# Performance work log

Measured on AMD Instinct MI355X. Metric: run time of the kernel, lower is better.

Reference implementation:

```python
import jax, jax.numpy as jnp
import numpy as np

# Graph sizes: each graph has exactly 32 nodes (forced by the rearrange + lin1 in_features)
BS = 4096
NODES = 32
N = BS * NODES          # 131072 total nodes
F_IN = 128
E_PER_G = 512
E = BS * E_PER_G        # 2097152 edges, all within-graph
HID = 1024
NCLS = 10


def setup_inputs() -> dict:
    key = jax.random.key(0)
    ks = jax.random.split(key, 9)
    x = jax.random.normal(ks[0], (N, F_IN), dtype=jnp.float32)
    # within-graph random edges: local node ids in [0,32) + per-graph offset
    graph_off = jnp.repeat(jnp.arange(BS, dtype=jnp.int64), E_PER_G) * NODES
    src = jax.random.randint(ks[1], (E,), 0, NODES, dtype=jnp.int64) + graph_off
    dst = jax.random.randint(ks[2], (E,), 0, NODES, dtype=jnp.int64) + graph_off
    edge_index = jnp.stack([src, dst], axis=0)
    s = 0.05
    gconv_w = jax.random.normal(ks[3], (F_IN, F_IN), dtype=jnp.float32) * s
    gconv_b = jax.random.normal(ks[4], (F_IN,), dtype=jnp.float32) * s
    lin1_w = jax.random.normal(ks[5], (HID, F_IN * NODES), dtype=jnp.float32) * s
    lin1_b = jax.random.normal(ks[6], (HID,), dtype=jnp.float32) * s
    lin2_w = jax.random.normal(ks[7], (NCLS, HID), dtype=jnp.float32) * s
    lin2_b = jax.random.normal(ks[8], (NCLS,), dtype=jnp.float32) * s
    return {"x": x, "edge_index": edge_index, "gconv_w": gconv_w,
            "gconv_b": gconv_b, "lin1_w": lin1_w, "lin1_b": lin1_b,
            "lin2_w": lin2_w, "lin2_b": lin2_b, "bs": BS}


def reference(x, edge_index, gconv_w, gconv_b, lin1_w, lin1_b, lin2_w, lin2_b, bs):
    # GINConv (eps=0): h_i = Linear( x_i + sum_{j->i} x_j )
    src, dst = edge_index[0], edge_index[1]
    agg = jax.ops.segment_sum(x[src], dst, num_segments=x.shape[0])  # [N, F]
    h = (x + agg) @ gconv_w.T + gconv_b                               # [N, F]
    h = jax.nn.relu(h)
    # rearrange '(bs e) f -> bs (f e)' with e=32 nodes per graph
    f = h.shape[-1]
    h = h.reshape(bs, NODES, f).transpose(0, 2, 1).reshape(bs, f * NODES)
    h = h @ lin1_w.T + lin1_b
    # dropout is identity in eval mode
    h = jax.nn.relu(h)
    h = h @ lin2_w.T + lin2_b
    return jax.nn.softmax(h, axis=-1)
```

## Files before the change

kernel.cpp:

```cpp
#include <hip/hip_runtime.h>

typedef _Float16 half_t;
typedef _Float16 halfv8 __attribute__((ext_vector_type(8)));
typedef _Float16 halfv4 __attribute__((ext_vector_type(4)));
typedef float    floatv4 __attribute__((ext_vector_type(4)));
typedef unsigned int uint;
typedef uint uintv4 __attribute__((ext_vector_type(4)));

#define NODES 32
#define FIN   128
#define EPG   512
#define NBS   4096
#define ETOT  (NBS*EPG)
#define HID   1024
#define KDIM  4096
#define NCLS  10
#define YP    36
#define WP    140

#define BM 256
#define BN 256
#define BK 64
#define KS 4
#define KSLEN (KDIM/KS)
#define NT (KSLEN/BK)

#define GLDS16(g, l)                                                        \
  __builtin_amdgcn_global_load_lds(                                         \
      (const __attribute__((address_space(1))) unsigned int*)(g),           \
      (__attribute__((address_space(3))) unsigned int*)(l), 16, 0, 0)

__global__ __launch_bounds__(256) void prep_cvt(const float* __restrict__ w1,
                                                half_t* __restrict__ w1p,
                                                const float* __restrict__ gw,
                                                half_t* __restrict__ gw16) {
  const size_t q = (size_t)blockIdx.x * 256 + threadIdx.x;
  const float* s;
  half_t* d;
  size_t off;
  if (q < 1048576) { s = w1; d = w1p; off = q; }
  else             { s = gw; d = gw16; off = q - 1048576; }
  floatv4 v = *(const floatv4*)(s + off * 4);
  halfv4 h = {(half_t)v[0], (half_t)v[1], (half_t)v[2], (half_t)v[3]};
  *(halfv4*)(d + off * 4) = h;
}

__global__ __launch_bounds__(256, 2) void gin_fused(
    const float* __restrict__ x, const int* __restrict__ ei,
    const half_t* __restrict__ gw16, const float* __restrict__ gb,
    half_t* __restrict__ H) {
  __shared__ __attribute__((aligned(16))) half_t Ws[FIN * WP];
  __shared__ __attribute__((aligned(16))) half_t Yt[4][FIN * YP];
  __shared__ uint cnt[4][512];

  const int t = threadIdx.x, w = t >> 6, l = t & 63;
  const int lr = l & 15, lk = l >> 4;
  const int g = blockIdx.x * 4 + w;

  const float* xg = x + (size_t)g * (NODES * FIN);
  floatv4 xr[2][4][2];
#pragma unroll
  for (int mt = 0; mt < 2; ++mt)
#pragma unroll
    for (int kk = 0; kk < 4; ++kk) {
      const float* p = xg + (mt * 16 + lr) * FIN + kk * 32 + lk * 8;
      xr[mt][kk][0] = *(const floatv4*)p;
      xr[mt][kk][1] = *(const floatv4*)(p + 4);
    }

  {
    const halfv8* gsrc = (const halfv8*)gw16;
#pragma unroll
    for (int i = 0; i < 8; ++i) {
      const int c = i * 256 + t;
      const int o = c >> 4, f8 = c & 15;
      *(halfv8*)&Ws[o * WP + f8 * 8] = gsrc[c];
    }
  }

  const int* sp = ei + (size_t)g * EPG;
  const int* dp = ei + (size_t)ETOT + (size_t)g * EPG;
  uintv4 s0 = *(const uintv4*)(sp + l * 8);
  uintv4 s1 = *(const uintv4*)(sp + l * 8 + 4);
  uintv4 d0 = *(const uintv4*)(dp + l * 8);
  uintv4 d1 = *(const uintv4*)(dp + l * 8 + 4);

  {
    uintv4* c4 = (uintv4*)cnt[w];
    uintv4 z = {0, 0, 0, 0};
    c4[l] = z;
    c4[l + 64] = z;
  }
#pragma unroll
  for (int q = 0; q < 4; ++q) {
    uint p0 = (d0[q] & 31) * 32 + (s0[q] & 31);
    atomicAdd(&cnt[w][p0 >> 1], 1u << ((p0 & 1) * 16));
    uint p1 = (d1[q] & 31) * 32 + (s1[q] & 31);
    atomicAdd(&cnt[w][p1 >> 1], 1u << ((p1 & 1) * 16));
  }

  halfv8 af[2][4];
#pragma unroll
  for (int mt = 0; mt < 2; ++mt)
#pragma unroll
    for (int kk = 0; kk < 4; ++kk) {
      halfv8 h;
#pragma unroll
      for (int q = 0; q < 4; ++q) {
        h[q]     = (half_t)xr[mt][kk][0][q];
        h[q + 4] = (half_t)xr[mt][kk][1][q];
      }
      af[mt][kk] = h;
    }

  __syncthreads();

  floatv4 acc[2][8] = {};
#pragma unroll
  for (int kk = 0; kk < 4; ++kk) {
    halfv8 bfk[8];
#pragma unroll
    for (int nt = 0; nt < 8; ++nt)
      bfk[nt] = *(const halfv8*)&Ws[(nt * 16 + lr) * WP + kk * 32 + lk * 8];
#pragma unroll
    for (int nt = 0; nt < 8; ++nt)
#pragma unroll
      for (int mt = 0; mt < 2; ++mt)
        acc[mt][nt] = __builtin_amdgcn_mfma_f32_16x16x32_f16(af[mt][kk], bfk[nt],
                                                             acc[mt][nt], 0, 0, 0);
  }
  __builtin_amdgcn_sched_barrier(0);

  half_t* yw = Yt[w];
#pragma unroll
  for (int mt = 0; mt < 2; ++mt)
#pragma unroll
    for (int nt = 0; nt < 8; ++nt) {
      halfv4 h = {(half_t)acc[mt][nt][0], (half_t)acc[mt][nt][1],
                  (half_t)acc[mt][nt][2], (half_t)acc[mt][nt][3]};
      *(halfv4*)&yw[(nt * 16 + lr) * YP + mt * 16 + lk * 4] = h;
    }

  const unsigned short* c16 = (const unsigned short*)cnt[w];
  halfv8 am[2];
#pragma unroll
  for (int mt = 0; mt < 2; ++mt) {
    const int i = mt * 16 + lr;
#pragma unroll
    for (int q = 0; q < 8; ++q) {
      const int j = lk * 8 + q;
      float c = (float)c16[i * 32 + j] + ((j == i) ? 1.f : 0.f);
      am[mt][q] = (half_t)c;
    }
  }

  floatv4 acc2[2][8] = {};
#pragma unroll
  for (int nt = 0; nt < 8; ++nt) {
    halfv8 bf = *(const halfv8*)&yw[(nt * 16 + lr) * YP + lk * 8];
#pragma unroll
    for (int mt = 0; mt < 2; ++mt)
      acc2[mt][nt] = __builtin_amdgcn_mfma_f32_16x16x32_f16(am[mt], bf,
                                                            acc2[mt][nt], 0, 0, 0);
  }
  __builtin_amdgcn_sched_barrier(0);

#pragma unroll
  for (int nt = 0; nt < 8; ++nt) {
    const float bias = gb[nt * 16 + lr];
#pragma unroll
    for (int mt = 0; mt < 2; ++mt) {
      halfv4 h;
#pragma unroll
      for (int q = 0; q < 4; ++q) {
        const float v = acc2[mt][nt][q] + bias;
        h[q] = (half_t)(v > 0.f ? v : 0.f);
      }
      *(halfv4*)&yw[(nt * 16 + lr) * YP + mt * 16 + lk * 4] = h;
    }
  }
  __builtin_amdgcn_sched_barrier(0);

  half_t* Hg = H + (size_t)g * KDIM;
#pragma unroll
  for (int c = 0; c < 8; ++c) {
    const int ch = c * 64 + l;
    const int o = ch >> 2, m0 = (ch & 3) * 8;
    halfv8 v = *(const halfv8*)&yw[o * YP + m0];
    *(halfv8*)(Hg + ch * 8) = v;
  }
}

__global__ __launch_bounds__(512, 2) void lin1_gemm(
    const half_t* __restrict__ A, const half_t* __restrict__ B,
    half_t* __restrict__ Cbase) {
  __shared__ __attribute__((aligned(16))) half_t As[2 * 2 * 8192];
  __shared__ __attribute__((aligned(16))) half_t Bs[2 * 2 * 8192];

  const int t = threadIdx.x;
  const int orig = blockIdx.x;
  const int wg = (orig & 7) * 32 + (orig >> 3);
  const int mt = wg & 15, rest = wg >> 4;
  const int nt_ = rest & 3, ksz = rest >> 2;
  const int m0 = mt * BM, n0 = nt_ * BN, k0 = ksz * KSLEN;

  const int srow0 = t >> 3, c_ = t & 7;
  const int cs0 = (c_ ^ (srow0 & 7)) * 8;
  const int srow1 = srow0 + 64;
  const int cs1 = (c_ ^ (srow1 & 7)) * 8;
  const half_t* gA[2][2] = {
      {A + (size_t)(m0 + srow0) * KDIM + k0 + cs0,
       A + (size_t)(m0 + srow1) * KDIM + k0 + cs1},
      {A + (size_t)(m0 + 128 + srow0) * KDIM + k0 + cs0,
       A + (size_t)(m0 + 128 + srow1) * KDIM + k0 + cs1}};
  const half_t* gB[2][2] = {
      {B + (size_t)(n0 + srow0) * KDIM + k0 + cs0,
       B + (size_t)(n0 + srow1) * KDIM + k0 + cs1},
      {B + (size_t)(n0 + 128 + srow0) * KDIM + k0 + cs0,
       B + (size_t)(n0 + 128 + srow1) * KDIM + k0 + cs1}};

#define STG_A(buf, hf, kk)                                                   \
  { GLDS16(gA[hf][0] + (kk) * BK, &As[(buf) * 16384 + (hf) * 8192 + t * 8]); \
    GLDS16(gA[hf][1] + (kk) * BK,                                            \
           &As[(buf) * 16384 + (hf) * 8192 + (t + 512) * 8]); }
#define STG_B(buf, hf, kk)                                                   \
  { GLDS16(gB[hf][0] + (kk) * BK, &Bs[(buf) * 16384 + (hf) * 8192 + t * 8]); \
    GLDS16(gB[hf][1] + (kk) * BK,                                            \
           &Bs[(buf) * 16384 + (hf) * 8192 + (t + 512) * 8]); }

  const int w = t >> 6, l = t & 63, lr = l & 15, lk = l >> 4;
  const int wm = (w >> 2) * 128, wn = (w & 3) * 64;
  const int ah = wm >> 7;
  const int bh = wn >> 7;
  const int bro = (wn & 64) + lr;
  const int rsw = lr & 7;

  floatv4 acc[8][4] = {};

  STG_B(0, 0, 0) STG_A(0, 0, 0) STG_A(0, 1, 0) STG_B(0, 1, 0)
  STG_B(1, 0, 1) STG_A(1, 0, 1)

  for (int kt = 0; kt < NT; ++kt) {
    const int cur = kt & 1, nxt = cur ^ 1;
    const int kA = (kt + 1) & 15, kB = (kt + 2) & 15;
    halfv8 af[4][2], bfA[2][2], bfB[2][2];

    asm volatile("s_waitcnt vmcnt(4)" ::: "memory");
    __builtin_amdgcn_s_barrier();
    __builtin_amdgcn_sched_barrier(0);
    STG_A(nxt, 1, kA)
#pragma unroll
    for (int mf = 0; mf < 4; ++mf)
#pragma unroll
      for (int ks = 0; ks < 2; ++ks)
        af[mf][ks] = *(const halfv8*)&As[cur * 16384 + ah * 8192 +
                                         (mf * 16 + lr) * 64 +
                                         (((ks * 4 + lk) ^ rsw) * 8)];
#pragma unroll
    for (int nf = 0; nf < 2; ++nf)
#pragma unroll
      for (int ks = 0; ks < 2; ++ks)
        bfA[nf][ks] = *(const halfv8*)&Bs[cur * 16384 + bh * 8192 +
                                          (bro + nf * 16) * 64 +
                                          (((ks * 4 + lk) ^ rsw) * 8)];
    __builtin_amdgcn_s_setprio(1);
#pragma unroll
    for (int mf = 0; mf < 4; ++mf)
#pragma unroll
      for (int nf = 0; nf < 2; ++nf)
#pragma unroll
        for (int ks = 0; ks < 2; ++ks)
          acc[mf][nf] = __builtin_amdgcn_mfma_f32_16x16x32_f16(
              af[mf][ks], bfA[nf][ks], acc[mf][nf], 0, 0, 0);
    __builtin_amdgcn_s_setprio(0);

    STG_B(nxt, 1, kA)
#pragma unroll
    for (int nf = 0; nf < 2; ++nf)
#pragma unroll
      for (int ks = 0; ks < 2; ++ks)
        bfB[nf][ks] = *(const halfv8*)&Bs[cur * 16384 + bh * 8192 +
                                          (bro + 32 + nf * 16) * 64 +
                                          (((ks * 4 + lk) ^ rsw) * 8)];
    __builtin_amdgcn_s_setprio(1);
#pragma unroll
    for (int mf = 0; mf < 4; ++mf)
#pragma unroll
      for (int nf = 0; nf < 2; ++nf)
#pragma unroll
        for (int ks = 0; ks < 2; ++ks)
          acc[mf][nf + 2] = __builtin_amdgcn_mfma_f32_16x16x32_f16(
              af[mf][ks], bfB[nf][ks], acc[mf][nf + 2], 0, 0, 0);
    __builtin_amdgcn_s_setprio(0);

    asm volatile("s_waitcnt lgkmcnt(0)" ::: "memory");
    __builtin_amdgcn_s_barrier();
    __builtin_amdgcn_sched_barrier(0);
    STG_B(cur, 0, kB)
#pragma unroll
    for (int mf = 0; mf < 4; ++mf)
#pragma unroll
      for (int ks = 0; ks < 2; ++ks)
        af[mf][ks] = *(const halfv8*)&As[cur * 16384 + ah * 8192 +
                                         (64 + mf * 16 + lr) * 64 +
                                         (((ks * 4 + lk) ^ rsw) * 8)];
    __builtin_amdgcn_s_setprio(1);
#pragma unroll
    for (int mf = 0; mf < 4; ++mf)
#pragma unroll
      for (int nf = 0; nf < 2; ++nf)
#pragma unroll
        for (int ks = 0; ks < 2; ++ks)
          acc[mf + 4][nf] = __builtin_amdgcn_mfma_f32_16x16x32_f16(
              af[mf][ks], bfA[nf][ks], acc[mf + 4][nf], 0, 0, 0);
    __builtin_amdgcn_s_setprio(0);

    asm volatile("s_waitcnt lgkmcnt(0)" ::: "memory");
    __builtin_amdgcn_s_barrier();
    __builtin_amdgcn_sched_barrier(0);
    STG_A(cur, 0, kB)
    __builtin_amdgcn_s_setprio(1);
#pragma unroll
    for (int mf = 0; mf < 4; ++mf)
#pragma unroll
      for (int nf = 0; nf < 2; ++nf)
#pragma unroll
        for (int ks = 0; ks < 2; ++ks)
          acc[mf + 4][nf + 2] = __builtin_amdgcn_mfma_f32_16x16x32_f16(
              af[mf][ks], bfB[nf][ks], acc[mf + 4][nf + 2], 0, 0, 0);
    __builtin_amdgcn_s_setprio(0);
  }

  half_t* C = Cbase + (size_t)ksz * ((size_t)NBS * HID);
#pragma unroll
  for (int mf = 0; mf < 8; ++mf)
#pragma unroll
    for (int nf = 0; nf < 4; ++nf) {
      const int n = n0 + wn + nf * 16 + lr;
#pragma unroll
      for (int q = 0; q < 4; ++q) {
        const int m = m0 + wm + mf * 16 + lk * 4 + q;
        C[(size_t)m * HID + n] = (half_t)acc[mf][nf][q];
      }
    }
#undef STG_A
#undef STG_B
}

__global__ __launch_bounds__(256) void head(
    const half_t* __restrict__ Cb, const float* __restrict__ b1,
    const float* __restrict__ w2, const float* __restrict__ b2,
    float* __restrict__ out) {
  __shared__ __attribute__((aligned(16))) float w2s[NCLS * HID];
  const int t = threadIdx.x;
  {
    const floatv4* s4 = (const floatv4*)w2;
    floatv4* d4 = (floatv4*)w2s;
    for (int i = t; i < (NCLS * HID) / 4; i += 256) d4[i] = s4[i];
  }
  __syncthreads();
  const int w = t >> 6, l = t & 63;
  const int row = blockIdx.x * 4 + w;

  float r[16];
#pragma unroll
  for (int jj = 0; jj < 4; ++jj) {
    floatv4 bb = *(const floatv4*)&b1[jj * 256 + l * 4];
    float s[4] = {bb[0], bb[1], bb[2], bb[3]};
#pragma unroll
    for (int p = 0; p < KS; ++p) {
      const half_t* cp = Cb + (size_t)p * ((size_t)NBS * HID) + (size_t)row * HID;
      halfv4 u = *(const halfv4*)&cp[jj * 256 + l * 4];
#pragma unroll
      for (int q = 0; q < 4; ++q) s[q] += (float)u[q];
    }
#pragma unroll
    for (int q = 0; q < 4; ++q) r[jj * 4 + q] = s[q] > 0.f ? s[q] : 0.f;
  }
  float lg[10];
#pragma unroll
  for (int c = 0; c < NCLS; ++c) {
    float p = 0.f;
#pragma unroll
    for (int jj = 0; jj < 4; ++jj) {
      floatv4 wv = *(const floatv4*)&w2s[c * HID + jj * 256 + l * 4];
      p += r[jj * 4 + 0] * wv[0] + r[jj * 4 + 1] * wv[1] +
           r[jj * 4 + 2] * wv[2] + r[jj * 4 + 3] * wv[3];
    }
#pragma unroll
    for (int off = 32; off >= 1; off >>= 1) p += __shfl_xor(p, off);
    lg[c] = p + b2[c];
  }
  float mx = lg[0];
#pragma unroll
  for (int c = 1; c < NCLS; ++c) mx = fmaxf(mx, lg[c]);
  float sum = 0.f;
#pragma unroll
  for (int c = 0; c < NCLS; ++c) { lg[c] = __expf(lg[c] - mx); sum += lg[c]; }
  const float inv = 1.f / sum;
  float myv = 0.f;
#pragma unroll
  for (int c = 0; c < NCLS; ++c) myv = (l == c) ? lg[c] * inv : myv;
  if (l < NCLS) out[(size_t)row * NCLS + l] = myv;
}

extern "C" void kernel_launch(void* const* d_in, const int* in_sizes, int n_in,
                              void* d_out, int out_size, void* d_ws, size_t ws_size,
                              hipStream_t stream) {
  (void)in_sizes; (void)n_in; (void)out_size; (void)ws_size;
  const float* x  = (const float*)d_in[0];
  const int*   ei = (const int*)d_in[1];
  const float* gw = (const float*)d_in[2];
  const float* gb = (const float*)d_in[3];
  const float* w1 = (const float*)d_in[4];
  const float* b1 = (const float*)d_in[5];
  const float* w2 = (const float*)d_in[6];
  const float* b2 = (const float*)d_in[7];
  float* out = (float*)d_out;

  char* ws = (char*)d_ws;
  half_t* H    = (half_t*)(ws);
  half_t* C    = (half_t*)(ws + 33554432);
  half_t* w1p  = (half_t*)(ws + 67108864);
  half_t* gw16 = (half_t*)(ws + 75497472);

  prep_cvt <<<dim3(4112),    dim3(256), 0, stream>>>(w1, w1p, gw, gw16);
  gin_fused<<<dim3(NBS / 4), dim3(256), 0, stream>>>(x, ei, gw16, gb, H);
  lin1_gemm<<<dim3(16 * 4 * KS), dim3(512), 0, stream>>>(H, w1p, C);
  head     <<<dim3(NBS / 4), dim3(256), 0, stream>>>(C, b1, w2, b2, out);
}
```

Baseline: 90.93 us.

## Restructure lin1 GEMM LDS layout and staging schedule into quarter-tile pipeline

```diff
diff --git a/kernel.cpp b/kernel.cpp
--- a/kernel.cpp
+++ b/kernel.cpp
@@ -29,6 +29,15 @@
   __builtin_amdgcn_global_load_lds(                                         \
       (const __attribute__((address_space(1))) unsigned int*)(g),           \
       (__attribute__((address_space(3))) unsigned int*)(l), 16, 0, 0)
+
+__device__ __forceinline__ int aidx(int r, int cc) {
+  return (r >> 7) * 8192 + ((r >> 6) & 1) * 4096 + (r & 63) * 64 +
+         ((cc ^ (r & 7)) * 8);
+}
+__device__ __forceinline__ int bidx(int r, int cc) {
+  return (r >> 7) * 8192 + ((r >> 5) & 1) * 4096 + ((r >> 6) & 1) * 2048 +
+         (r & 31) * 64 + ((cc ^ (r & 7)) * 8);
+}
 
 __global__ __launch_bounds__(256) void prep_cvt(const float* __restrict__ w1,
                                                 half_t* __restrict__ w1p,
@@ -194,8 +203,8 @@
 __global__ __launch_bounds__(512, 2) void lin1_gemm(
     const half_t* __restrict__ A, const half_t* __restrict__ B,
     half_t* __restrict__ Cbase) {
-  __shared__ __attribute__((aligned(16))) half_t As[2 * 2 * 8192];
-  __shared__ __attribute__((aligned(16))) half_t Bs[2 * 2 * 8192];
+  __shared__ __attribute__((aligned(16))) half_t As[2][16384];
+  __shared__ __attribute__((aligned(16))) half_t Bs[2][16384];
 
   const int t = threadIdx.x;
   const int orig = blockIdx.x;
@@ -204,65 +213,54 @@
   const int nt_ = rest & 3, ksz = rest >> 2;
   const int m0 = mt * BM, n0 = nt_ * BN, k0 = ksz * KSLEN;
 
-  const int srow0 = t >> 3, c_ = t & 7;
-  const int cs0 = (c_ ^ (srow0 & 7)) * 8;
-  const int srow1 = srow0 + 64;
-  const int cs1 = (c_ ^ (srow1 & 7)) * 8;
-  const half_t* gA[2][2] = {
-      {A + (size_t)(m0 + srow0) * KDIM + k0 + cs0,
-       A + (size_t)(m0 + srow1) * KDIM + k0 + cs1},
-      {A + (size_t)(m0 + 128 + srow0) * KDIM + k0 + cs0,
-       A + (size_t)(m0 + 128 + srow1) * KDIM + k0 + cs1}};
-  const half_t* gB[2][2] = {
-      {B + (size_t)(n0 + srow0) * KDIM + k0 + cs0,
-       B + (size_t)(n0 + srow1) * KDIM + k0 + cs1},
-      {B + (size_t)(n0 + 128 + srow0) * KDIM + k0 + cs0,
-       B + (size_t)(n0 + 128 + srow1) * KDIM + k0 + cs1}};
-
-#define STG_A(buf, hf, kk)                                                   \
-  { GLDS16(gA[hf][0] + (kk) * BK, &As[(buf) * 16384 + (hf) * 8192 + t * 8]); \
-    GLDS16(gA[hf][1] + (kk) * BK,                                            \
-           &As[(buf) * 16384 + (hf) * 8192 + (t + 512) * 8]); }
-#define STG_B(buf, hf, kk)                                                   \
-  { GLDS16(gB[hf][0] + (kk) * BK, &Bs[(buf) * 16384 + (hf) * 8192 + t * 8]); \
-    GLDS16(gB[hf][1] + (kk) * BK,                                            \
-           &Bs[(buf) * 16384 + (hf) * 8192 + (t + 512) * 8]); }
+  const int csw = ((t & 7) ^ ((t >> 3) & 7)) * 8;
+  const int ar0 = t >> 3;
+  const int brl = (t >> 3) & 31, bg = t >> 8;
+  const half_t* pA[2][2];
+  const half_t* pB[2][2];
+#pragma unroll
+  for (int h = 0; h < 2; ++h) {
+    pA[h][0] = A + (size_t)(m0 + ar0 + h * 64) * KDIM + k0 + csw;
+    pA[h][1] = pA[h][0] + (size_t)128 * KDIM;
+    pB[h][0] = B + (size_t)(n0 + bg * 64 + h * 32 + brl) * KDIM + k0 + csw;
+    pB[h][1] = pB[h][0] + (size_t)128 * KDIM;
+  }
+
+#define STG_A(buf, h, kt_)                                                   \
+  { GLDS16(pA[h][0] + (kt_) * BK, &As[buf][(h) * 4096 + t * 8]);             \
+    GLDS16(pA[h][1] + (kt_) * BK, &As[buf][8192 + (h) * 4096 + t * 8]); }
+#define STG_B(buf, h, kt_)                                                   \
+  { GLDS16(pB[h][0] + (kt_) * BK, &Bs[buf][(h) * 4096 + t * 8]);             \
+    GLDS16(pB[h][1] + (kt_) * BK, &Bs[buf][8192 + (h) * 4096 + t * 8]); }
 
   const int w = t >> 6, l = t & 63, lr = l & 15, lk = l >> 4;
   const int wm = (w >> 2) * 128, wn = (w & 3) * 64;
-  const int ah = wm >> 7;
-  const int bh = wn >> 7;
-  const int bro = (wn & 64) + lr;
-  const int rsw = lr & 7;
 
   floatv4 acc[8][4] = {};
 
-  STG_B(0, 0, 0) STG_A(0, 0, 0) STG_A(0, 1, 0) STG_B(0, 1, 0)
-  STG_B(1, 0, 1) STG_A(1, 0, 1)
+  STG_A(0, 0, 0) STG_B(0, 0, 0) STG_B(0, 1, 0) STG_A(0, 1, 0)
+  asm volatile("s_waitcnt vmcnt(4)" ::: "memory");
+  __builtin_amdgcn_s_barrier();
 
   for (int kt = 0; kt < NT; ++kt) {
     const int cur = kt & 1, nxt = cur ^ 1;
-    const int kA = (kt + 1) & 15, kB = (kt + 2) & 15;
-    halfv8 af[4][2], bfA[2][2], bfB[2][2];
-
-    asm volatile("s_waitcnt vmcnt(4)" ::: "memory");
-    __builtin_amdgcn_s_barrier();
+    const int ktn = (kt + 1 < NT) ? (kt + 1) : 0;
+    halfv8 af[4][2], bfL[2][2], bfH[2][2];
+
+#pragma unroll
+    for (int mf = 0; mf < 4; ++mf)
+#pragma unroll
+      for (int ks = 0; ks < 2; ++ks)
+        af[mf][ks] = *(const halfv8*)&As[cur][aidx(wm + mf * 16 + lr, ks * 4 + lk)];
+#pragma unroll
+    for (int nf = 0; nf < 2; ++nf)
+#pragma unroll
+      for (int ks = 0; ks < 2; ++ks)
+        bfL[nf][ks] = *(const halfv8*)&Bs[cur][bidx(wn + nf * 16 + lr, ks * 4 + lk)];
+    STG_A(nxt, 0, ktn)
+    __builtin_amdgcn_s_barrier();
+    asm volatile("s_waitcnt lgkmcnt(0)" ::: "memory");
     __builtin_amdgcn_sched_barrier(0);
-    STG_A(nxt, 1, kA)
-#pragma unroll
-    for (int mf = 0; mf < 4; ++mf)
-#pragma unroll
-      for (int ks = 0; ks < 2; ++ks)
-        af[mf][ks] = *(const halfv8*)&As[cur * 16384 + ah * 8192 +
-                                         (mf * 16 + lr) * 64 +
-                                         (((ks * 4 + lk) ^ rsw) * 8)];
-#pragma unroll
-    for (int nf = 0; nf < 2; ++nf)
-#pragma unroll
-      for (int ks = 0; ks < 2; ++ks)
-        bfA[nf][ks] = *(const halfv8*)&Bs[cur * 16384 + bh * 8192 +
-                                          (bro + nf * 16) * 64 +
-                                          (((ks * 4 + lk) ^ rsw) * 8)];
     __builtin_amdgcn_s_setprio(1);
 #pragma unroll
     for (int mf = 0; mf < 4; ++mf)
@@ -271,17 +269,20 @@
 #pragma unroll
         for (int ks = 0; ks < 2; ++ks)
           acc[mf][nf] = __builtin_amdgcn_mfma_f32_16x16x32_f16(
-              af[mf][ks], bfA[nf][ks], acc[mf][nf], 0, 0, 0);
+              af[mf][ks], bfL[nf][ks], acc[mf][nf], 0, 0, 0);
     __builtin_amdgcn_s_setprio(0);
-
-    STG_B(nxt, 1, kA)
+    asm volatile("s_waitcnt vmcnt(4)" ::: "memory");
+    __builtin_amdgcn_s_barrier();
+
 #pragma unroll
     for (int nf = 0; nf < 2; ++nf)
 #pragma unroll
       for (int ks = 0; ks < 2; ++ks)
-        bfB[nf][ks] = *(const halfv8*)&Bs[cur * 16384 + bh * 8192 +
-                                          (bro + 32 + nf * 16) * 64 +
-                                          (((ks * 4 + lk) ^ rsw) * 8)];
+        bfH[nf][ks] = *(const halfv8*)&Bs[cur][bidx(wn + 32 + nf * 16 + lr, ks * 4 + lk)];
+    STG_B(nxt, 0, ktn)
+    __builtin_amdgcn_s_barrier();
+    asm volatile("s_waitcnt lgkmcnt(0)" ::: "memory");
+    __builtin_amdgcn_sched_barrier(0);
     __builtin_amdgcn_s_setprio(1);
 #pragma unroll
     for (int mf = 0; mf < 4; ++mf)
@@ -290,20 +291,20 @@
 #pragma unroll
         for (int ks = 0; ks < 2; ++ks)
           acc[mf][nf + 2] = __builtin_amdgcn_mfma_f32_16x16x32_f16(
-              af[mf][ks], bfB[nf][ks], acc[mf][nf + 2], 0, 0, 0);
+              af[mf][ks], bfH[nf][ks], acc[mf][nf + 2], 0, 0, 0);
     __builtin_amdgcn_s_setprio(0);
-
+    asm volatile("s_waitcnt vmcnt(4)" ::: "memory");
+    __builtin_amdgcn_s_barrier();
+
+#pragma unroll
+    for (int mf = 0; mf < 4; ++mf)
+#pragma unroll
+      for (int ks = 0; ks < 2; ++ks)
+        af[mf][ks] = *(const halfv8*)&As[cur][aidx(wm + 64 + mf * 16 + lr, ks * 4 + lk)];
+    STG_B(nxt, 1, ktn)
+    __builtin_amdgcn_s_barrier();
     asm volatile("s_waitcnt lgkmcnt(0)" ::: "memory");
-    __builtin_amdgcn_s_barrier();
     __builtin_amdgcn_sched_barrier(0);
-    STG_B(cur, 0, kB)
-#pragma unroll
-    for (int mf = 0; mf < 4; ++mf)
-#pragma unroll
-      for (int ks = 0; ks < 2; ++ks)
-        af[mf][ks] = *(const halfv8*)&As[cur * 16384 + ah * 8192 +
-                                         (64 + mf * 16 + lr) * 64 +
-                                         (((ks * 4 + lk) ^ rsw) * 8)];
     __builtin_amdgcn_s_setprio(1);
 #pragma unroll
     for (int mf = 0; mf < 4; ++mf)
@@ -312,13 +313,13 @@
 #pragma unroll
         for (int ks = 0; ks < 2; ++ks)
           acc[mf + 4][nf] = __builtin_amdgcn_mfma_f32_16x16x32_f16(
-              af[mf][ks], bfA[nf][ks], acc[mf + 4][nf], 0, 0, 0);
+              af[mf][ks], bfL[nf][ks], acc[mf + 4][nf], 0, 0, 0);
     __builtin_amdgcn_s_setprio(0);
-
-    asm volatile("s_waitcnt lgkmcnt(0)" ::: "memory");
+    __builtin_amdgcn_s_barrier();
+
+    STG_A(nxt, 1, ktn)
     __builtin_amdgcn_s_barrier();
     __builtin_amdgcn_sched_barrier(0);
-    STG_A(cur, 0, kB)
     __builtin_amdgcn_s_setprio(1);
 #pragma unroll
     for (int mf = 0; mf < 4; ++mf)
@@ -327,8 +328,10 @@
 #pragma unroll
         for (int ks = 0; ks < 2; ++ks)
           acc[mf + 4][nf + 2] = __builtin_amdgcn_mfma_f32_16x16x32_f16(
-              af[mf][ks], bfB[nf][ks], acc[mf + 4][nf + 2], 0, 0, 0);
+              af[mf][ks], bfH[nf][ks], acc[mf + 4][nf + 2], 0, 0, 0);
     __builtin_amdgcn_s_setprio(0);
+    asm volatile("s_waitcnt vmcnt(4)" ::: "memory");
+    __builtin_amdgcn_s_barrier();
   }
 
   half_t* C = Cbase + (size_t)ksz * ((size_t)NBS * HID);
```

New measurement: 81.03 us (median of 4 runs). -10.9%, faster.
